# Optimization experiments

Measured on AMD Instinct MI355X. Metric: run time of the kernel, lower is better.

## Reference

```python
import jax, jax.numpy as jnp
import numpy as np

B, L, HP, H, W = 4, 32, 32, 64, 64
D, DFFN, MAXL = 32, 64, 128

def setup_inputs() -> dict:
    key = jax.random.key(0)
    ks = jax.random.split(key, 20)
    rn = lambda k, s, sc=0.1: jax.random.normal(k, s, jnp.float32) * sc
    return {
        'x': jax.random.normal(ks[0], (B, 2 * L * HP, H, W), jnp.float32),
        'in_proj_w': rn(ks[1], (D, 12)), 'in_proj_b': rn(ks[2], (D,)),
        'layer_emb': rn(ks[3], (MAXL, D)),
        'time_decay': rn(ks[4], (D,)), 'time_first': rn(ks[5], (D,)),
        'ln_tm_g': jnp.ones((D,)), 'ln_tm_b': jnp.zeros((D,)),
        'tm_r': rn(ks[6], (D, D)), 'tm_k': rn(ks[7], (D, D)),
        'tm_v': rn(ks[8], (D, D)), 'tm_out': rn(ks[9], (D, D)),
        'ln_cm_g': jnp.ones((D,)), 'ln_cm_b': jnp.zeros((D,)),
        'cm_k': rn(ks[10], (DFFN, D)), 'cm_v': rn(ks[11], (D, DFFN)), 'cm_r': rn(ks[12], (D, D)),
        'gate_w': rn(ks[13], (1, D)), 'gate_b': rn(ks[14], (1,)),
        'row_w': rn(ks[15], (H, D)), 'row_b': rn(ks[16], (H,)),
        'col_w': rn(ks[17], (W, D)), 'col_b': rn(ks[18], (W,)),
    }

def _ln(x, g, b, eps=1e-5):
    mu = x.mean(-1, keepdims=True)
    var = ((x - mu) ** 2).mean(-1, keepdims=True)
    return (x - mu) * jax.lax.rsqrt(var + eps) * g + b

def _stats(a, b):
    # a, b: [B, L, HP, H, W] -> [B, L, HP, 12]
    af = a.reshape(*a.shape[:-2], -1)
    bf = b.reshape(*b.shape[:-2], -1)
    hs = lambda f: jnp.stack([f.mean(-1), f.std(-1, ddof=1), f.min(-1), f.max(-1)], -1)
    d = af - bf
    dm = d.mean(-1, keepdims=True)
    ds = d.std(-1, ddof=1, keepdims=True)
    dl2 = jnp.linalg.norm(d, axis=-1, keepdims=True)
    na = jnp.maximum(jnp.linalg.norm(af, axis=-1), 1e-8)
    nb = jnp.maximum(jnp.linalg.norm(bf, axis=-1), 1e-8)
    cos = ((af * bf).sum(-1) / (na * nb))[..., None]
    return jnp.concatenate([hs(af), hs(bf), dm, ds, dl2, cos], -1)

def reference(x, in_proj_w, in_proj_b, layer_emb, time_decay, time_first,
              ln_tm_g, ln_tm_b, tm_r, tm_k, tm_v, tm_out,
              ln_cm_g, ln_cm_b, cm_k, cm_v, cm_r,
              gate_w, gate_b, row_w, row_b, col_w, col_b):
    n = L * HP
    a = x[:, :n].reshape(B, L, HP, H, W)
    b = x[:, n:].reshape(B, L, HP, H, W)
    stats = _stats(a, b)                                   # [B,L,HP,12]
    feat_in = jnp.einsum('blhs,ds->blhd', stats, in_proj_w) + in_proj_b \
        + layer_emb[:L][None, :, None, :]
    feat_in = jnp.transpose(feat_in, (1, 0, 2, 3))         # [L,B,HP,D]
    wdec = jnp.exp(time_decay)

    def step(state, f):
        aa, bb, pp = state
        xn = _ln(f, ln_tm_g, ln_tm_b)
        r = jax.nn.sigmoid(xn @ tm_r.T)
        k = xn @ tm_k.T
        v = xn @ tm_v.T
        ww = time_first + k
        p = jnp.maximum(pp, ww)
        e1 = jnp.exp(pp - p)
        e2 = jnp.exp(ww - p)
        wkv = (e1 * aa + e2 * v) / jnp.maximum(e1 * bb + e2, 1e-8)
        ww2 = pp - wdec
        p2 = jnp.maximum(ww2, k)
        e1b = jnp.exp(ww2 - p2)
        e2b = jnp.exp(k - p2)
        y = f + r * (wkv @ tm_out.T)
        xn2 = _ln(y, ln_cm_g, ln_cm_b)
        kk = jnp.square(jax.nn.relu(xn2 @ cm_k.T))
        y = y + jax.nn.sigmoid(xn2 @ cm_r.T) * (kk @ cm_v.T)
        return (e1b * aa + e2b * v, e1b * bb + e2b, p2), y

    z = jnp.zeros((B, HP, D), x.dtype)
    init = (z, z, jnp.full((B, HP, D), -1e30, x.dtype))
    _, feats = jax.lax.scan(step, init, feat_in)           # [L,B,HP,D]

    gate = feats @ gate_w.T + gate_b                       # [L,B,HP,1]
    row = feats @ row_w.T + row_b                          # [L,B,HP,H]
    col = feats @ col_w.T + col_b                          # [L,B,HP,W]
    mask = jax.nn.sigmoid(gate[..., None] + row[..., None] + col[..., None, :])
    aT = jnp.transpose(a, (1, 0, 2, 3, 4))
    bT = jnp.transpose(b, (1, 0, 2, 3, 4))
    merged = mask * aT + (1.0 - mask) * bT                 # [L,B,HP,H,W]
    mixed = jnp.transpose(merged, (1, 0, 2, 3, 4)).reshape(B, n, H, W)
    return mixed, jax.nn.sigmoid(gate).mean(), mask.mean()
```

## Files before the change

### kernel.cpp

```cpp
#include <hip/hip_runtime.h>
#include <math.h>


__device__ __forceinline__ float sigf(float v) { return 1.0f / (1.0f + __expf(-v)); }

__device__ __forceinline__ float bl(float v, int l) {
    return __int_as_float(__builtin_amdgcn_readlane(__float_as_int(v), l));
}

__global__ __launch_bounds__(256) void k_stats(
    const float* __restrict__ x, const float* __restrict__ in_proj_w,
    const float* __restrict__ in_proj_b, const float* __restrict__ layer_emb,
    float* __restrict__ feat)
{
    __shared__ float red[4][9];
    __shared__ float tot[9];
    const int bid = blockIdx.x;
    const int hp = bid & 31, l = (bid >> 5) & 31, bb = bid >> 10;
    const float4* pa = (const float4*)(x + (size_t)(bb * 2048 + l * 32 + hp) * 4096);
    const float4* pb = (const float4*)(x + (size_t)(bb * 2048 + 1024 + l * 32 + hp) * 4096);
    const int t = threadIdx.x;

    float sa = 0.f, saa = 0.f, sb = 0.f, sbb = 0.f, sab = 0.f;
    float mna = 3.4e38f, mxa = -3.4e38f, mnb = 3.4e38f, mxb = -3.4e38f;
#pragma unroll
    for (int it = 0; it < 4; ++it) {
        float4 a4 = pa[t + it * 256];
        float4 b4 = pb[t + it * 256];
        sa  += a4.x + a4.y + a4.z + a4.w;
        sb  += b4.x + b4.y + b4.z + b4.w;
        saa += a4.x * a4.x + a4.y * a4.y + a4.z * a4.z + a4.w * a4.w;
        sbb += b4.x * b4.x + b4.y * b4.y + b4.z * b4.z + b4.w * b4.w;
        sab += a4.x * b4.x + a4.y * b4.y + a4.z * b4.z + a4.w * b4.w;
        mna = fminf(mna, fminf(fminf(a4.x, a4.y), fminf(a4.z, a4.w)));
        mxa = fmaxf(mxa, fmaxf(fmaxf(a4.x, a4.y), fmaxf(a4.z, a4.w)));
        mnb = fminf(mnb, fminf(fminf(b4.x, b4.y), fminf(b4.z, b4.w)));
        mxb = fmaxf(mxb, fmaxf(fmaxf(b4.x, b4.y), fmaxf(b4.z, b4.w)));
    }
#pragma unroll
    for (int m = 1; m < 64; m <<= 1) {
        sa  += __shfl_xor(sa, m);
        saa += __shfl_xor(saa, m);
        sb  += __shfl_xor(sb, m);
        sbb += __shfl_xor(sbb, m);
        sab += __shfl_xor(sab, m);
        mna = fminf(mna, __shfl_xor(mna, m));
        mxa = fmaxf(mxa, __shfl_xor(mxa, m));
        mnb = fminf(mnb, __shfl_xor(mnb, m));
        mxb = fmaxf(mxb, __shfl_xor(mxb, m));
    }
    const int lane = t & 63, wv = t >> 6;
    if (lane == 0) {
        red[wv][0] = sa;  red[wv][1] = saa; red[wv][2] = sb;  red[wv][3] = sbb;
        red[wv][4] = sab; red[wv][5] = mna; red[wv][6] = mxa; red[wv][7] = mnb;
        red[wv][8] = mxb;
    }
    __syncthreads();
    if (t == 0) {
#pragma unroll
        for (int q = 0; q < 5; ++q) tot[q] = red[0][q] + red[1][q] + red[2][q] + red[3][q];
        tot[5] = fminf(fminf(red[0][5], red[1][5]), fminf(red[2][5], red[3][5]));
        tot[6] = fmaxf(fmaxf(red[0][6], red[1][6]), fmaxf(red[2][6], red[3][6]));
        tot[7] = fminf(fminf(red[0][7], red[1][7]), fminf(red[2][7], red[3][7]));
        tot[8] = fmaxf(fmaxf(red[0][8], red[1][8]), fmaxf(red[2][8], red[3][8]));
    }
    __syncthreads();
    if (t < 32) {
        const float SA = tot[0], SAA = tot[1], SB = tot[2], SBB = tot[3], SAB = tot[4];
        const float inv_n = 1.f / 4096.f, inv_nm1 = 1.f / 4095.f;
        float st[12];
        st[0] = SA * inv_n;
        st[1] = sqrtf(fmaxf(SAA - SA * SA * inv_n, 0.f) * inv_nm1);
        st[2] = tot[5]; st[3] = tot[6];
        st[4] = SB * inv_n;
        st[5] = sqrtf(fmaxf(SBB - SB * SB * inv_n, 0.f) * inv_nm1);
        st[6] = tot[7]; st[7] = tot[8];
        const float SD = SA - SB, SDD = SAA - 2.f * SAB + SBB;
        st[8]  = SD * inv_n;
        st[9]  = sqrtf(fmaxf(SDD - SD * SD * inv_n, 0.f) * inv_nm1);
        st[10] = sqrtf(fmaxf(SDD, 0.f));
        const float na = fmaxf(sqrtf(SAA), 1e-8f), nb2 = fmaxf(sqrtf(SBB), 1e-8f);
        st[11] = SAB / (na * nb2);
        float acc = in_proj_b[t] + layer_emb[l * 32 + t];
#pragma unroll
        for (int s2 = 0; s2 < 12; ++s2) acc += st[s2] * in_proj_w[t * 12 + s2];
        feat[((l * 4 + bb) * 32 + hp) * 32 + t] = acc;
    }
}

__global__ __launch_bounds__(64, 1) void k_scan(
    const float* __restrict__ feat,
    const float* __restrict__ time_decay, const float* __restrict__ time_first,
    const float* __restrict__ ln_tm_g, const float* __restrict__ ln_tm_b,
    const float* __restrict__ tm_r, const float* __restrict__ tm_k,
    const float* __restrict__ tm_v, const float* __restrict__ tm_out,
    const float* __restrict__ ln_cm_g, const float* __restrict__ ln_cm_b,
    const float* __restrict__ cm_k, const float* __restrict__ cm_v,
    const float* __restrict__ cm_r, float* __restrict__ feats_out)
{
    const int t = threadIdx.x;
    const int d = t & 31;

    float w_r[32], w_k[32], w_v[32], w_o[32], w_cr[32], w_ck[32], w_cv[64];
    {
        const float4* pr = (const float4*)(tm_r  + d * 32);
        const float4* pk = (const float4*)(tm_k  + d * 32);
        const float4* pv = (const float4*)(tm_v  + d * 32);
        const float4* po = (const float4*)(tm_out + d * 32);
        const float4* pc = (const float4*)(cm_r  + d * 32);
        const float4* pq = (const float4*)(cm_k  + t * 32);
        const float4* pw = (const float4*)(cm_v  + d * 64);
#pragma unroll
        for (int jq = 0; jq < 8; ++jq) {
            float4 v;
            v = pr[jq]; w_r[4*jq] = v.x; w_r[4*jq+1] = v.y; w_r[4*jq+2] = v.z; w_r[4*jq+3] = v.w;
            v = pk[jq]; w_k[4*jq] = v.x; w_k[4*jq+1] = v.y; w_k[4*jq+2] = v.z; w_k[4*jq+3] = v.w;
            v = pv[jq]; w_v[4*jq] = v.x; w_v[4*jq+1] = v.y; w_v[4*jq+2] = v.z; w_v[4*jq+3] = v.w;
            v = po[jq]; w_o[4*jq] = v.x; w_o[4*jq+1] = v.y; w_o[4*jq+2] = v.z; w_o[4*jq+3] = v.w;
            v = pc[jq]; w_cr[4*jq] = v.x; w_cr[4*jq+1] = v.y; w_cr[4*jq+2] = v.z; w_cr[4*jq+3] = v.w;
            v = pq[jq]; w_ck[4*jq] = v.x; w_ck[4*jq+1] = v.y; w_ck[4*jq+2] = v.z; w_ck[4*jq+3] = v.w;
        }
#pragma unroll
        for (int jq = 0; jq < 16; ++jq) {
            float4 v = pw[jq];
            w_cv[4*jq] = v.x; w_cv[4*jq+1] = v.y; w_cv[4*jq+2] = v.z; w_cv[4*jq+3] = v.w;
        }
    }
    const float gt = ln_tm_g[d], bt = ln_tm_b[d];
    const float gc = ln_cm_g[d], bc = ln_cm_b[d];
    const float tf = time_first[d];
    const float wd = __expf(time_decay[d]);
    const int seq = blockIdx.x;
    const int bb = seq >> 5, hp = seq & 31;
    const int base = (bb * 32 + hp) * 32 + d;

    float aa = 0.f, bbs = 0.f, pp = -1e30f;
    float f = feat[base];

    for (int l = 0; l < 32; ++l) {
        float fnext = 0.f;
        if (l < 31) fnext = feat[base + (l + 1) * 4096];
        float s = f, q = f * f;
#pragma unroll
        for (int m = 1; m < 32; m <<= 1) { s += __shfl_xor(s, m, 32); q += __shfl_xor(q, m, 32); }
        const float mu = s * (1.f / 32.f);
        const float var = fmaxf(q * (1.f / 32.f) - mu * mu, 0.f);
        const float xn = (f - mu) * rsqrtf(var + 1e-5f) * gt + bt;
        float racc = 0.f, kacc = 0.f, vacc = 0.f;
#pragma unroll
        for (int j = 0; j < 32; ++j) {
            const float xj = bl(xn, j);
            racc += xj * w_r[j];
            kacc += xj * w_k[j];
            vacc += xj * w_v[j];
        }
        const float r = sigf(racc);
        const float k = kacc, v = vacc;
        const float ww = tf + k;
        const float p = fmaxf(pp, ww);
        const float e1 = __expf(pp - p), e2 = __expf(ww - p);
        const float wkv = (e1 * aa + e2 * v) / fmaxf(e1 * bbs + e2, 1e-8f);
        const float ww2 = pp - wd;
        const float p2 = fmaxf(ww2, k);
        const float e1b = __expf(ww2 - p2), e2b = __expf(k - p2);
        aa = e1b * aa + e2b * v;
        bbs = e1b * bbs + e2b;
        pp = p2;
        float oacc = 0.f;
#pragma unroll
        for (int j = 0; j < 32; ++j) oacc += bl(wkv, j) * w_o[j];
        const float y = f + r * oacc;
        float s2 = y, q2 = y * y;
#pragma unroll
        for (int m = 1; m < 32; m <<= 1) { s2 += __shfl_xor(s2, m, 32); q2 += __shfl_xor(q2, m, 32); }
        const float mu2 = s2 * (1.f / 32.f);
        const float var2 = fmaxf(q2 * (1.f / 32.f) - mu2 * mu2, 0.f);
        const float xn2 = (y - mu2) * rsqrtf(var2 + 1e-5f) * gc + bc;
        float ck = 0.f, cracc = 0.f;
#pragma unroll
        for (int j = 0; j < 32; ++j) {
            const float xj = bl(xn2, j);
            ck    += xj * w_ck[j];
            cracc += xj * w_cr[j];
        }
        float kkv = fmaxf(ck, 0.f);
        kkv *= kkv;
        float cv0 = 0.f, cv1 = 0.f;
#pragma unroll
        for (int e = 0; e < 64; e += 2) {
            cv0 += bl(kkv, e)     * w_cv[e];
            cv1 += bl(kkv, e + 1) * w_cv[e + 1];
        }
        const float y2 = y + sigf(cracc) * (cv0 + cv1);
        if (t < 32) feats_out[base + l * 4096] = y2;
        f = fnext;
    }
}

__global__ __launch_bounds__(256) void k_merge(
    const float* __restrict__ x, const float* __restrict__ feats,
    const float* __restrict__ gate_w, const float* __restrict__ gate_b,
    const float* __restrict__ row_w, const float* __restrict__ row_b,
    const float* __restrict__ col_w, const float* __restrict__ col_b,
    float* __restrict__ out, float* __restrict__ gpart, float* __restrict__ mpart)
{
    __shared__ float fs[32];
    __shared__ float row_s[64], col_s[64];
    __shared__ float gate_sh;
    __shared__ float red[4];
    const int bid = blockIdx.x;
    const int hp = bid & 31, l = (bid >> 5) & 31, bb = bid >> 10;
    const int t = threadIdx.x;

    if (t < 32) fs[t] = feats[((l * 4 + bb) * 32 + hp) * 32 + t];
    __syncthreads();
    if (t < 64) {
        float acc = row_b[t];
#pragma unroll
        for (int d2 = 0; d2 < 32; ++d2) acc += fs[d2] * row_w[t * 32 + d2];
        row_s[t] = acc;
    } else if (t < 128) {
        const int w = t - 64;
        float acc = col_b[w];
#pragma unroll
        for (int d2 = 0; d2 < 32; ++d2) acc += fs[d2] * col_w[w * 32 + d2];
        col_s[w] = acc;
    } else if (t == 128) {
        float acc = gate_b[0];
#pragma unroll
        for (int d2 = 0; d2 < 32; ++d2) acc += fs[d2] * gate_w[d2];
        gate_sh = acc;
    }
    __syncthreads();
    const float gate = gate_sh;
    const float4* pa = (const float4*)(x + (size_t)(bb * 2048 + l * 32 + hp) * 4096);
    const float4* pb = (const float4*)(x + (size_t)(bb * 2048 + 1024 + l * 32 + hp) * 4096);
    float4* po = (float4*)(out + (size_t)(bb * 1024 + l * 32 + hp) * 4096);

    float msum = 0.f;
#pragma unroll
    for (int it = 0; it < 4; ++it) {
        const int i = t + it * 256;
        const float4 a4 = pa[i];
        const float4 b4 = pb[i];
        const int h = i >> 4, w0 = (i & 15) * 4;
        const float gr = gate + row_s[h];
        const float m0 = sigf(gr + col_s[w0 + 0]);
        const float m1 = sigf(gr + col_s[w0 + 1]);
        const float m2 = sigf(gr + col_s[w0 + 2]);
        const float m3 = sigf(gr + col_s[w0 + 3]);
        float4 o;
        o.x = b4.x + m0 * (a4.x - b4.x);
        o.y = b4.y + m1 * (a4.y - b4.y);
        o.z = b4.z + m2 * (a4.z - b4.z);
        o.w = b4.w + m3 * (a4.w - b4.w);
        po[i] = o;
        msum += m0 + m1 + m2 + m3;
    }
#pragma unroll
    for (int m = 1; m < 64; m <<= 1) msum += __shfl_xor(msum, m);
    if ((t & 63) == 0) red[t >> 6] = msum;
    __syncthreads();
    if (t == 0) {
        mpart[bid] = red[0] + red[1] + red[2] + red[3];
        gpart[bid] = sigf(gate);
    }
}

__global__ __launch_bounds__(256) void k_final(
    const float* __restrict__ gpart, const float* __restrict__ mpart,
    float* __restrict__ out)
{
    __shared__ float rg[4], rm[4];
    const int t = threadIdx.x;
    float gs = 0.f, ms = 0.f;
    for (int i = t; i < 4096; i += 256) { gs += gpart[i]; ms += mpart[i]; }
#pragma unroll
    for (int m = 1; m < 64; m <<= 1) { gs += __shfl_xor(gs, m); ms += __shfl_xor(ms, m); }
    if ((t & 63) == 0) { rg[t >> 6] = gs; rm[t >> 6] = ms; }
    __syncthreads();
    if (t == 0) {
        out[16777216] = (rg[0] + rg[1] + rg[2] + rg[3]) * (1.f / 4096.f);
        out[16777217] = (rm[0] + rm[1] + rm[2] + rm[3]) * (1.f / 16777216.f);
    }
}

extern "C" void kernel_launch(void* const* d_in, const int* in_sizes, int n_in,
                              void* d_out, int out_size, void* d_ws, size_t ws_size,
                              hipStream_t stream) {
    const float* x          = (const float*)d_in[0];
    const float* in_proj_w  = (const float*)d_in[1];
    const float* in_proj_b  = (const float*)d_in[2];
    const float* layer_emb  = (const float*)d_in[3];
    const float* time_decay = (const float*)d_in[4];
    const float* time_first = (const float*)d_in[5];
    const float* ln_tm_g    = (const float*)d_in[6];
    const float* ln_tm_b    = (const float*)d_in[7];
    const float* tm_r       = (const float*)d_in[8];
    const float* tm_k       = (const float*)d_in[9];
    const float* tm_v       = (const float*)d_in[10];
    const float* tm_out     = (const float*)d_in[11];
    const float* ln_cm_g    = (const float*)d_in[12];
    const float* ln_cm_b    = (const float*)d_in[13];
    const float* cm_k       = (const float*)d_in[14];
    const float* cm_v       = (const float*)d_in[15];
    const float* cm_r       = (const float*)d_in[16];
    const float* gate_w     = (const float*)d_in[17];
    const float* gate_b     = (const float*)d_in[18];
    const float* row_w      = (const float*)d_in[19];
    const float* row_b      = (const float*)d_in[20];
    const float* col_w      = (const float*)d_in[21];
    const float* col_b      = (const float*)d_in[22];
    float* out = (float*)d_out;

    float* wsf   = (float*)d_ws;
    float* feat  = wsf;
    float* fy    = wsf + 131072;
    float* gpart = wsf + 262144;
    float* mpart = wsf + 266240;

    k_stats<<<dim3(4096), dim3(256), 0, stream>>>(x, in_proj_w, in_proj_b, layer_emb, feat);
    k_scan<<<dim3(128), dim3(64), 0, stream>>>(feat, time_decay, time_first,
                                               ln_tm_g, ln_tm_b, tm_r, tm_k, tm_v, tm_out,
                                               ln_cm_g, ln_cm_b, cm_k, cm_v, cm_r, fy);
    k_merge<<<dim3(4096), dim3(256), 0, stream>>>(x, fy, gate_w, gate_b,
                                                  row_w, row_b, col_w, col_b,
                                                  out, gpart, mpart);
    k_final<<<dim3(1), dim3(256), 0, stream>>>(gpart, mpart, out);
}
```

Measured before the change: 336.5 us.

## Fuse all stages into one persistent kernel with grid-wide atomic barriers

Replaces the four launches (stats, scan, merge, final) with one persistent kernel of 256 blocks. Blocks loop over work items and synchronise through atomic-counter grid barriers, so launch gaps disappear. The scan stage now packs four sequences per block, one per wave, and splits its dot products into four independent accumulators for more ILP. The costs are fewer resident blocks for the memory-bound stats and merge phases, spin-wait barrier overhead, and an extra memset to reset the counters.

```diff
diff --git a/kernel.cpp b/kernel.cpp
--- a/kernel.cpp
+++ b/kernel.cpp
@@ -2,286 +2,334 @@
 #include <math.h>
 
 
+#define NBLK 256
+
 __device__ __forceinline__ float sigf(float v) { return 1.0f / (1.0f + __expf(-v)); }
-
 __device__ __forceinline__ float bl(float v, int l) {
     return __int_as_float(__builtin_amdgcn_readlane(__float_as_int(v), l));
 }
 
-__global__ __launch_bounds__(256) void k_stats(
+__device__ __forceinline__ void gbar(unsigned* c) {
+    __threadfence();
+    __syncthreads();
+    if (threadIdx.x == 0) {
+        __hip_atomic_fetch_add(c, 1u, __ATOMIC_ACQ_REL, __HIP_MEMORY_SCOPE_AGENT);
+        while (__hip_atomic_load(c, __ATOMIC_ACQUIRE, __HIP_MEMORY_SCOPE_AGENT) < NBLK)
+            __builtin_amdgcn_s_sleep(1);
+    }
+    __syncthreads();
+    __threadfence();
+}
+
+__global__ __launch_bounds__(256, 1) void k_fused(
     const float* __restrict__ x, const float* __restrict__ in_proj_w,
     const float* __restrict__ in_proj_b, const float* __restrict__ layer_emb,
-    float* __restrict__ feat)
-{
-    __shared__ float red[4][9];
-    __shared__ float tot[9];
-    const int bid = blockIdx.x;
-    const int hp = bid & 31, l = (bid >> 5) & 31, bb = bid >> 10;
-    const float4* pa = (const float4*)(x + (size_t)(bb * 2048 + l * 32 + hp) * 4096);
-    const float4* pb = (const float4*)(x + (size_t)(bb * 2048 + 1024 + l * 32 + hp) * 4096);
-    const int t = threadIdx.x;
-
-    float sa = 0.f, saa = 0.f, sb = 0.f, sbb = 0.f, sab = 0.f;
-    float mna = 3.4e38f, mxa = -3.4e38f, mnb = 3.4e38f, mxb = -3.4e38f;
-#pragma unroll
-    for (int it = 0; it < 4; ++it) {
-        float4 a4 = pa[t + it * 256];
-        float4 b4 = pb[t + it * 256];
-        sa  += a4.x + a4.y + a4.z + a4.w;
-        sb  += b4.x + b4.y + b4.z + b4.w;
-        saa += a4.x * a4.x + a4.y * a4.y + a4.z * a4.z + a4.w * a4.w;
-        sbb += b4.x * b4.x + b4.y * b4.y + b4.z * b4.z + b4.w * b4.w;
-        sab += a4.x * b4.x + a4.y * b4.y + a4.z * b4.z + a4.w * b4.w;
-        mna = fminf(mna, fminf(fminf(a4.x, a4.y), fminf(a4.z, a4.w)));
-        mxa = fmaxf(mxa, fmaxf(fmaxf(a4.x, a4.y), fmaxf(a4.z, a4.w)));
-        mnb = fminf(mnb, fminf(fminf(b4.x, b4.y), fminf(b4.z, b4.w)));
-        mxb = fmaxf(mxb, fmaxf(fmaxf(b4.x, b4.y), fmaxf(b4.z, b4.w)));
-    }
-#pragma unroll
-    for (int m = 1; m < 64; m <<= 1) {
-        sa  += __shfl_xor(sa, m);
-        saa += __shfl_xor(saa, m);
-        sb  += __shfl_xor(sb, m);
-        sbb += __shfl_xor(sbb, m);
-        sab += __shfl_xor(sab, m);
-        mna = fminf(mna, __shfl_xor(mna, m));
-        mxa = fmaxf(mxa, __shfl_xor(mxa, m));
-        mnb = fminf(mnb, __shfl_xor(mnb, m));
-        mxb = fmaxf(mxb, __shfl_xor(mxb, m));
-    }
-    const int lane = t & 63, wv = t >> 6;
-    if (lane == 0) {
-        red[wv][0] = sa;  red[wv][1] = saa; red[wv][2] = sb;  red[wv][3] = sbb;
-        red[wv][4] = sab; red[wv][5] = mna; red[wv][6] = mxa; red[wv][7] = mnb;
-        red[wv][8] = mxb;
-    }
-    __syncthreads();
-    if (t == 0) {
-#pragma unroll
-        for (int q = 0; q < 5; ++q) tot[q] = red[0][q] + red[1][q] + red[2][q] + red[3][q];
-        tot[5] = fminf(fminf(red[0][5], red[1][5]), fminf(red[2][5], red[3][5]));
-        tot[6] = fmaxf(fmaxf(red[0][6], red[1][6]), fmaxf(red[2][6], red[3][6]));
-        tot[7] = fminf(fminf(red[0][7], red[1][7]), fminf(red[2][7], red[3][7]));
-        tot[8] = fmaxf(fmaxf(red[0][8], red[1][8]), fmaxf(red[2][8], red[3][8]));
-    }
-    __syncthreads();
-    if (t < 32) {
-        const float SA = tot[0], SAA = tot[1], SB = tot[2], SBB = tot[3], SAB = tot[4];
-        const float inv_n = 1.f / 4096.f, inv_nm1 = 1.f / 4095.f;
-        float st[12];
-        st[0] = SA * inv_n;
-        st[1] = sqrtf(fmaxf(SAA - SA * SA * inv_n, 0.f) * inv_nm1);
-        st[2] = tot[5]; st[3] = tot[6];
-        st[4] = SB * inv_n;
-        st[5] = sqrtf(fmaxf(SBB - SB * SB * inv_n, 0.f) * inv_nm1);
-        st[6] = tot[7]; st[7] = tot[8];
-        const float SD = SA - SB, SDD = SAA - 2.f * SAB + SBB;
-        st[8]  = SD * inv_n;
-        st[9]  = sqrtf(fmaxf(SDD - SD * SD * inv_n, 0.f) * inv_nm1);
-        st[10] = sqrtf(fmaxf(SDD, 0.f));
-        const float na = fmaxf(sqrtf(SAA), 1e-8f), nb2 = fmaxf(sqrtf(SBB), 1e-8f);
-        st[11] = SAB / (na * nb2);
-        float acc = in_proj_b[t] + layer_emb[l * 32 + t];
-#pragma unroll
-        for (int s2 = 0; s2 < 12; ++s2) acc += st[s2] * in_proj_w[t * 12 + s2];
-        feat[((l * 4 + bb) * 32 + hp) * 32 + t] = acc;
-    }
-}
-
-__global__ __launch_bounds__(64, 1) void k_scan(
-    const float* __restrict__ feat,
     const float* __restrict__ time_decay, const float* __restrict__ time_first,
     const float* __restrict__ ln_tm_g, const float* __restrict__ ln_tm_b,
     const float* __restrict__ tm_r, const float* __restrict__ tm_k,
     const float* __restrict__ tm_v, const float* __restrict__ tm_out,
     const float* __restrict__ ln_cm_g, const float* __restrict__ ln_cm_b,
     const float* __restrict__ cm_k, const float* __restrict__ cm_v,
-    const float* __restrict__ cm_r, float* __restrict__ feats_out)
-{
-    const int t = threadIdx.x;
-    const int d = t & 31;
-
-    float w_r[32], w_k[32], w_v[32], w_o[32], w_cr[32], w_ck[32], w_cv[64];
-    {
-        const float4* pr = (const float4*)(tm_r  + d * 32);
-        const float4* pk = (const float4*)(tm_k  + d * 32);
-        const float4* pv = (const float4*)(tm_v  + d * 32);
-        const float4* po = (const float4*)(tm_out + d * 32);
-        const float4* pc = (const float4*)(cm_r  + d * 32);
-        const float4* pq = (const float4*)(cm_k  + t * 32);
-        const float4* pw = (const float4*)(cm_v  + d * 64);
-#pragma unroll
-        for (int jq = 0; jq < 8; ++jq) {
-            float4 v;
-            v = pr[jq]; w_r[4*jq] = v.x; w_r[4*jq+1] = v.y; w_r[4*jq+2] = v.z; w_r[4*jq+3] = v.w;
-            v = pk[jq]; w_k[4*jq] = v.x; w_k[4*jq+1] = v.y; w_k[4*jq+2] = v.z; w_k[4*jq+3] = v.w;
-            v = pv[jq]; w_v[4*jq] = v.x; w_v[4*jq+1] = v.y; w_v[4*jq+2] = v.z; w_v[4*jq+3] = v.w;
-            v = po[jq]; w_o[4*jq] = v.x; w_o[4*jq+1] = v.y; w_o[4*jq+2] = v.z; w_o[4*jq+3] = v.w;
-            v = pc[jq]; w_cr[4*jq] = v.x; w_cr[4*jq+1] = v.y; w_cr[4*jq+2] = v.z; w_cr[4*jq+3] = v.w;
-            v = pq[jq]; w_ck[4*jq] = v.x; w_ck[4*jq+1] = v.y; w_ck[4*jq+2] = v.z; w_ck[4*jq+3] = v.w;
-        }
-#pragma unroll
-        for (int jq = 0; jq < 16; ++jq) {
-            float4 v = pw[jq];
-            w_cv[4*jq] = v.x; w_cv[4*jq+1] = v.y; w_cv[4*jq+2] = v.z; w_cv[4*jq+3] = v.w;
-        }
-    }
-    const float gt = ln_tm_g[d], bt = ln_tm_b[d];
-    const float gc = ln_cm_g[d], bc = ln_cm_b[d];
-    const float tf = time_first[d];
-    const float wd = __expf(time_decay[d]);
-    const int seq = blockIdx.x;
-    const int bb = seq >> 5, hp = seq & 31;
-    const int base = (bb * 32 + hp) * 32 + d;
-
-    float aa = 0.f, bbs = 0.f, pp = -1e30f;
-    float f = feat[base];
-
-    for (int l = 0; l < 32; ++l) {
-        float fnext = 0.f;
-        if (l < 31) fnext = feat[base + (l + 1) * 4096];
-        float s = f, q = f * f;
-#pragma unroll
-        for (int m = 1; m < 32; m <<= 1) { s += __shfl_xor(s, m, 32); q += __shfl_xor(q, m, 32); }
-        const float mu = s * (1.f / 32.f);
-        const float var = fmaxf(q * (1.f / 32.f) - mu * mu, 0.f);
-        const float xn = (f - mu) * rsqrtf(var + 1e-5f) * gt + bt;
-        float racc = 0.f, kacc = 0.f, vacc = 0.f;
-#pragma unroll
-        for (int j = 0; j < 32; ++j) {
-            const float xj = bl(xn, j);
-            racc += xj * w_r[j];
-            kacc += xj * w_k[j];
-            vacc += xj * w_v[j];
-        }
-        const float r = sigf(racc);
-        const float k = kacc, v = vacc;
-        const float ww = tf + k;
-        const float p = fmaxf(pp, ww);
-        const float e1 = __expf(pp - p), e2 = __expf(ww - p);
-        const float wkv = (e1 * aa + e2 * v) / fmaxf(e1 * bbs + e2, 1e-8f);
-        const float ww2 = pp - wd;
-        const float p2 = fmaxf(ww2, k);
-        const float e1b = __expf(ww2 - p2), e2b = __expf(k - p2);
-        aa = e1b * aa + e2b * v;
-        bbs = e1b * bbs + e2b;
-        pp = p2;
-        float oacc = 0.f;
-#pragma unroll
-        for (int j = 0; j < 32; ++j) oacc += bl(wkv, j) * w_o[j];
-        const float y = f + r * oacc;
-        float s2 = y, q2 = y * y;
-#pragma unroll
-        for (int m = 1; m < 32; m <<= 1) { s2 += __shfl_xor(s2, m, 32); q2 += __shfl_xor(q2, m, 32); }
-        const float mu2 = s2 * (1.f / 32.f);
-        const float var2 = fmaxf(q2 * (1.f / 32.f) - mu2 * mu2, 0.f);
-        const float xn2 = (y - mu2) * rsqrtf(var2 + 1e-5f) * gc + bc;
-        float ck = 0.f, cracc = 0.f;
-#pragma unroll
-        for (int j = 0; j < 32; ++j) {
-            const float xj = bl(xn2, j);
-            ck    += xj * w_ck[j];
-            cracc += xj * w_cr[j];
-        }
-        float kkv = fmaxf(ck, 0.f);
-        kkv *= kkv;
-        float cv0 = 0.f, cv1 = 0.f;
-#pragma unroll
-        for (int e = 0; e < 64; e += 2) {
-            cv0 += bl(kkv, e)     * w_cv[e];
-            cv1 += bl(kkv, e + 1) * w_cv[e + 1];
-        }
-        const float y2 = y + sigf(cracc) * (cv0 + cv1);
-        if (t < 32) feats_out[base + l * 4096] = y2;
-        f = fnext;
-    }
-}
-
-__global__ __launch_bounds__(256) void k_merge(
-    const float* __restrict__ x, const float* __restrict__ feats,
+    const float* __restrict__ cm_r,
     const float* __restrict__ gate_w, const float* __restrict__ gate_b,
     const float* __restrict__ row_w, const float* __restrict__ row_b,
     const float* __restrict__ col_w, const float* __restrict__ col_b,
-    float* __restrict__ out, float* __restrict__ gpart, float* __restrict__ mpart)
+    float* __restrict__ out, float* __restrict__ wsf)
 {
-    __shared__ float fs[32];
-    __shared__ float row_s[64], col_s[64];
-    __shared__ float gate_sh;
-    __shared__ float red[4];
+    float* feat  = wsf;
+    float* fy    = wsf + 131072;
+    float* gpart = wsf + 262144;
+    float* mpart = wsf + 262400;
+    unsigned* cnt = (unsigned*)(wsf + 262656);
+
     const int bid = blockIdx.x;
-    const int hp = bid & 31, l = (bid >> 5) & 31, bb = bid >> 10;
-    const int t = threadIdx.x;
-
-    if (t < 32) fs[t] = feats[((l * 4 + bb) * 32 + hp) * 32 + t];
-    __syncthreads();
-    if (t < 64) {
-        float acc = row_b[t];
-#pragma unroll
-        for (int d2 = 0; d2 < 32; ++d2) acc += fs[d2] * row_w[t * 32 + d2];
-        row_s[t] = acc;
-    } else if (t < 128) {
-        const int w = t - 64;
-        float acc = col_b[w];
-#pragma unroll
-        for (int d2 = 0; d2 < 32; ++d2) acc += fs[d2] * col_w[w * 32 + d2];
-        col_s[w] = acc;
-    } else if (t == 128) {
-        float acc = gate_b[0];
-#pragma unroll
-        for (int d2 = 0; d2 < 32; ++d2) acc += fs[d2] * gate_w[d2];
-        gate_sh = acc;
-    }
-    __syncthreads();
-    const float gate = gate_sh;
-    const float4* pa = (const float4*)(x + (size_t)(bb * 2048 + l * 32 + hp) * 4096);
-    const float4* pb = (const float4*)(x + (size_t)(bb * 2048 + 1024 + l * 32 + hp) * 4096);
-    float4* po = (float4*)(out + (size_t)(bb * 1024 + l * 32 + hp) * 4096);
-
-    float msum = 0.f;
-#pragma unroll
-    for (int it = 0; it < 4; ++it) {
-        const int i = t + it * 256;
-        const float4 a4 = pa[i];
-        const float4 b4 = pb[i];
-        const int h = i >> 4, w0 = (i & 15) * 4;
-        const float gr = gate + row_s[h];
-        const float m0 = sigf(gr + col_s[w0 + 0]);
-        const float m1 = sigf(gr + col_s[w0 + 1]);
-        const float m2 = sigf(gr + col_s[w0 + 2]);
-        const float m3 = sigf(gr + col_s[w0 + 3]);
-        float4 o;
-        o.x = b4.x + m0 * (a4.x - b4.x);
-        o.y = b4.y + m1 * (a4.y - b4.y);
-        o.z = b4.z + m2 * (a4.z - b4.z);
-        o.w = b4.w + m3 * (a4.w - b4.w);
-        po[i] = o;
-        msum += m0 + m1 + m2 + m3;
-    }
-#pragma unroll
-    for (int m = 1; m < 64; m <<= 1) msum += __shfl_xor(msum, m);
-    if ((t & 63) == 0) red[t >> 6] = msum;
-    __syncthreads();
-    if (t == 0) {
-        mpart[bid] = red[0] + red[1] + red[2] + red[3];
-        gpart[bid] = sigf(gate);
-    }
-}
-
-__global__ __launch_bounds__(256) void k_final(
-    const float* __restrict__ gpart, const float* __restrict__ mpart,
-    float* __restrict__ out)
-{
-    __shared__ float rg[4], rm[4];
-    const int t = threadIdx.x;
-    float gs = 0.f, ms = 0.f;
-    for (int i = t; i < 4096; i += 256) { gs += gpart[i]; ms += mpart[i]; }
-#pragma unroll
-    for (int m = 1; m < 64; m <<= 1) { gs += __shfl_xor(gs, m); ms += __shfl_xor(ms, m); }
-    if ((t & 63) == 0) { rg[t >> 6] = gs; rm[t >> 6] = ms; }
-    __syncthreads();
-    if (t == 0) {
-        out[16777216] = (rg[0] + rg[1] + rg[2] + rg[3]) * (1.f / 4096.f);
-        out[16777217] = (rm[0] + rm[1] + rm[2] + rm[3]) * (1.f / 16777216.f);
+    const int t   = threadIdx.x;
+
+    {
+        __shared__ float red[4][9];
+        __shared__ float tot[9];
+        for (int it16 = 0; it16 < 16; ++it16) {
+            const int g = bid + (it16 << 8);
+            const int hp = g & 31, l = (g >> 5) & 31, bb = g >> 10;
+            const float4* pa = (const float4*)(x + (size_t)(bb * 2048 + l * 32 + hp) * 4096);
+            const float4* pb = (const float4*)(x + (size_t)(bb * 2048 + 1024 + l * 32 + hp) * 4096);
+
+            float sa = 0.f, saa = 0.f, sb = 0.f, sbb = 0.f, sab = 0.f;
+            float mna = 3.4e38f, mxa = -3.4e38f, mnb = 3.4e38f, mxb = -3.4e38f;
+#pragma unroll
+            for (int it = 0; it < 4; ++it) {
+                float4 a4 = pa[t + it * 256];
+                float4 b4 = pb[t + it * 256];
+                sa  += a4.x + a4.y + a4.z + a4.w;
+                sb  += b4.x + b4.y + b4.z + b4.w;
+                saa += a4.x * a4.x + a4.y * a4.y + a4.z * a4.z + a4.w * a4.w;
+                sbb += b4.x * b4.x + b4.y * b4.y + b4.z * b4.z + b4.w * b4.w;
+                sab += a4.x * b4.x + a4.y * b4.y + a4.z * b4.z + a4.w * b4.w;
+                mna = fminf(mna, fminf(fminf(a4.x, a4.y), fminf(a4.z, a4.w)));
+                mxa = fmaxf(mxa, fmaxf(fmaxf(a4.x, a4.y), fmaxf(a4.z, a4.w)));
+                mnb = fminf(mnb, fminf(fminf(b4.x, b4.y), fminf(b4.z, b4.w)));
+                mxb = fmaxf(mxb, fmaxf(fmaxf(b4.x, b4.y), fmaxf(b4.z, b4.w)));
+            }
+#pragma unroll
+            for (int m = 1; m < 64; m <<= 1) {
+                sa  += __shfl_xor(sa, m);
+                saa += __shfl_xor(saa, m);
+                sb  += __shfl_xor(sb, m);
+                sbb += __shfl_xor(sbb, m);
+                sab += __shfl_xor(sab, m);
+                mna = fminf(mna, __shfl_xor(mna, m));
+                mxa = fmaxf(mxa, __shfl_xor(mxa, m));
+                mnb = fminf(mnb, __shfl_xor(mnb, m));
+                mxb = fmaxf(mxb, __shfl_xor(mxb, m));
+            }
+            const int lane = t & 63, wv = t >> 6;
+            if (lane == 0) {
+                red[wv][0] = sa;  red[wv][1] = saa; red[wv][2] = sb;  red[wv][3] = sbb;
+                red[wv][4] = sab; red[wv][5] = mna; red[wv][6] = mxa; red[wv][7] = mnb;
+                red[wv][8] = mxb;
+            }
+            __syncthreads();
+            if (t == 0) {
+#pragma unroll
+                for (int q = 0; q < 5; ++q) tot[q] = red[0][q] + red[1][q] + red[2][q] + red[3][q];
+                tot[5] = fminf(fminf(red[0][5], red[1][5]), fminf(red[2][5], red[3][5]));
+                tot[6] = fmaxf(fmaxf(red[0][6], red[1][6]), fmaxf(red[2][6], red[3][6]));
+                tot[7] = fminf(fminf(red[0][7], red[1][7]), fminf(red[2][7], red[3][7]));
+                tot[8] = fmaxf(fmaxf(red[0][8], red[1][8]), fmaxf(red[2][8], red[3][8]));
+            }
+            __syncthreads();
+            if (t < 32) {
+                const float SA = tot[0], SAA = tot[1], SB = tot[2], SBB = tot[3], SAB = tot[4];
+                const float inv_n = 1.f / 4096.f, inv_nm1 = 1.f / 4095.f;
+                float st[12];
+                st[0] = SA * inv_n;
+                st[1] = sqrtf(fmaxf(SAA - SA * SA * inv_n, 0.f) * inv_nm1);
+                st[2] = tot[5]; st[3] = tot[6];
+                st[4] = SB * inv_n;
+                st[5] = sqrtf(fmaxf(SBB - SB * SB * inv_n, 0.f) * inv_nm1);
+                st[6] = tot[7]; st[7] = tot[8];
+                const float SD = SA - SB, SDD = SAA - 2.f * SAB + SBB;
+                st[8]  = SD * inv_n;
+                st[9]  = sqrtf(fmaxf(SDD - SD * SD * inv_n, 0.f) * inv_nm1);
+                st[10] = sqrtf(fmaxf(SDD, 0.f));
+                const float na = fmaxf(sqrtf(SAA), 1e-8f), nb2 = fmaxf(sqrtf(SBB), 1e-8f);
+                st[11] = SAB / (na * nb2);
+                float acc = in_proj_b[t] + layer_emb[l * 32 + t];
+#pragma unroll
+                for (int s2 = 0; s2 < 12; ++s2) acc += st[s2] * in_proj_w[t * 12 + s2];
+                feat[((l * 4 + bb) * 32 + hp) * 32 + t] = acc;
+            }
+            __syncthreads();
+        }
+    }
+    gbar(&cnt[0]);
+
+    if (bid < 32) {
+        const int lane = t & 63;
+        const int d = lane & 31;
+        const int wv = t >> 6;
+        const int seq = bid * 4 + wv;
+        const int bb = seq >> 5, hp = seq & 31;
+
+        float w_r[32], w_k[32], w_v[32], w_o[32], w_cr[32], w_ck[32], w_cv[64];
+        {
+            const float4* pr = (const float4*)(tm_r  + d * 32);
+            const float4* pk = (const float4*)(tm_k  + d * 32);
+            const float4* pv = (const float4*)(tm_v  + d * 32);
+            const float4* po = (const float4*)(tm_out + d * 32);
+            const float4* pc = (const float4*)(cm_r  + d * 32);
+            const float4* pq = (const float4*)(cm_k  + lane * 32);
+            const float4* pw = (const float4*)(cm_v  + d * 64);
+#pragma unroll
+            for (int jq = 0; jq < 8; ++jq) {
+                float4 v;
+                v = pr[jq]; w_r[4*jq] = v.x; w_r[4*jq+1] = v.y; w_r[4*jq+2] = v.z; w_r[4*jq+3] = v.w;
+                v = pk[jq]; w_k[4*jq] = v.x; w_k[4*jq+1] = v.y; w_k[4*jq+2] = v.z; w_k[4*jq+3] = v.w;
+                v = pv[jq]; w_v[4*jq] = v.x; w_v[4*jq+1] = v.y; w_v[4*jq+2] = v.z; w_v[4*jq+3] = v.w;
+                v = po[jq]; w_o[4*jq] = v.x; w_o[4*jq+1] = v.y; w_o[4*jq+2] = v.z; w_o[4*jq+3] = v.w;
+                v = pc[jq]; w_cr[4*jq] = v.x; w_cr[4*jq+1] = v.y; w_cr[4*jq+2] = v.z; w_cr[4*jq+3] = v.w;
+                v = pq[jq]; w_ck[4*jq] = v.x; w_ck[4*jq+1] = v.y; w_ck[4*jq+2] = v.z; w_ck[4*jq+3] = v.w;
+            }
+#pragma unroll
+            for (int jq = 0; jq < 16; ++jq) {
+                float4 v = pw[jq];
+                w_cv[4*jq] = v.x; w_cv[4*jq+1] = v.y; w_cv[4*jq+2] = v.z; w_cv[4*jq+3] = v.w;
+            }
+        }
+        const float gt = ln_tm_g[d], bt = ln_tm_b[d];
+        const float gc = ln_cm_g[d], bc = ln_cm_b[d];
+        const float tf = time_first[d];
+        const float wd = __expf(time_decay[d]);
+        const int base = (bb * 32 + hp) * 32 + d;
+
+        float aa = 0.f, bbs = 0.f, pp = -1e30f;
+        float f = feat[base];
+
+        for (int l = 0; l < 32; ++l) {
+            float fnext = 0.f;
+            if (l < 31) fnext = feat[base + (l + 1) * 4096];
+            float s = f, q = f * f;
+#pragma unroll
+            for (int m = 1; m < 32; m <<= 1) { s += __shfl_xor(s, m, 32); q += __shfl_xor(q, m, 32); }
+            const float mu = s * (1.f / 32.f);
+            const float var = fmaxf(q * (1.f / 32.f) - mu * mu, 0.f);
+            const float xn = (f - mu) * rsqrtf(var + 1e-5f) * gt + bt;
+            float r0 = 0.f, r1 = 0.f, r2 = 0.f, r3 = 0.f;
+            float k0 = 0.f, k1 = 0.f, k2 = 0.f, k3 = 0.f;
+            float v0 = 0.f, v1 = 0.f, v2 = 0.f, v3 = 0.f;
+#pragma unroll
+            for (int j = 0; j < 8; ++j) {
+                const float x0 = bl(xn, j), x1 = bl(xn, j + 8), x2 = bl(xn, j + 16), x3 = bl(xn, j + 24);
+                r0 += x0 * w_r[j];      r1 += x1 * w_r[j + 8];
+                r2 += x2 * w_r[j + 16]; r3 += x3 * w_r[j + 24];
+                k0 += x0 * w_k[j];      k1 += x1 * w_k[j + 8];
+                k2 += x2 * w_k[j + 16]; k3 += x3 * w_k[j + 24];
+                v0 += x0 * w_v[j];      v1 += x1 * w_v[j + 8];
+                v2 += x2 * w_v[j + 16]; v3 += x3 * w_v[j + 24];
+            }
+            const float r = sigf((r0 + r1) + (r2 + r3));
+            const float k = (k0 + k1) + (k2 + k3);
+            const float v = (v0 + v1) + (v2 + v3);
+            const float ww = tf + k;
+            const float p = fmaxf(pp, ww);
+            const float e1 = __expf(pp - p), e2 = __expf(ww - p);
+            const float wkv = (e1 * aa + e2 * v) / fmaxf(e1 * bbs + e2, 1e-8f);
+            const float ww2 = pp - wd;
+            const float p2 = fmaxf(ww2, k);
+            const float e1b = __expf(ww2 - p2), e2b = __expf(k - p2);
+            aa = e1b * aa + e2b * v;
+            bbs = e1b * bbs + e2b;
+            pp = p2;
+            float o0 = 0.f, o1 = 0.f, o2 = 0.f, o3 = 0.f;
+#pragma unroll
+            for (int j = 0; j < 8; ++j) {
+                o0 += bl(wkv, j)      * w_o[j];
+                o1 += bl(wkv, j + 8)  * w_o[j + 8];
+                o2 += bl(wkv, j + 16) * w_o[j + 16];
+                o3 += bl(wkv, j + 24) * w_o[j + 24];
+            }
+            const float y = f + r * ((o0 + o1) + (o2 + o3));
+            float s2 = y, q2 = y * y;
+#pragma unroll
+            for (int m = 1; m < 32; m <<= 1) { s2 += __shfl_xor(s2, m, 32); q2 += __shfl_xor(q2, m, 32); }
+            const float mu2 = s2 * (1.f / 32.f);
+            const float var2 = fmaxf(q2 * (1.f / 32.f) - mu2 * mu2, 0.f);
+            const float xn2 = (y - mu2) * rsqrtf(var2 + 1e-5f) * gc + bc;
+            float c0 = 0.f, c1 = 0.f, c2 = 0.f, c3 = 0.f;
+            float g0 = 0.f, g1 = 0.f, g2 = 0.f, g3 = 0.f;
+#pragma unroll
+            for (int j = 0; j < 8; ++j) {
+                const float x0 = bl(xn2, j), x1 = bl(xn2, j + 8), x2 = bl(xn2, j + 16), x3 = bl(xn2, j + 24);
+                c0 += x0 * w_ck[j];      c1 += x1 * w_ck[j + 8];
+                c2 += x2 * w_ck[j + 16]; c3 += x3 * w_ck[j + 24];
+                g0 += x0 * w_cr[j];      g1 += x1 * w_cr[j + 8];
+                g2 += x2 * w_cr[j + 16]; g3 += x3 * w_cr[j + 24];
+            }
+            float kkv = fmaxf((c0 + c1) + (c2 + c3), 0.f);
+            kkv *= kkv;
+            const float cr = sigf((g0 + g1) + (g2 + g3));
+            float u0 = 0.f, u1 = 0.f, u2 = 0.f, u3 = 0.f;
+#pragma unroll
+            for (int e = 0; e < 16; ++e) {
+                u0 += bl(kkv, e)      * w_cv[e];
+                u1 += bl(kkv, e + 16) * w_cv[e + 16];
+                u2 += bl(kkv, e + 32) * w_cv[e + 32];
+                u3 += bl(kkv, e + 48) * w_cv[e + 48];
+            }
+            const float y2 = y + cr * ((u0 + u1) + (u2 + u3));
+            if (lane < 32) fy[base + l * 4096] = y2;
+            f = fnext;
+        }
+    }
+    gbar(&cnt[1]);
+
+    {
+        __shared__ float fs[32];
+        __shared__ float row_s[64], col_s[64];
+        __shared__ float gate_sh;
+        float msum = 0.f, gsum = 0.f;
+        for (int it16 = 0; it16 < 16; ++it16) {
+            const int g = bid + (it16 << 8);
+            const int hp = g & 31, l = (g >> 5) & 31, bb = g >> 10;
+            if (t < 32) fs[t] = fy[((l * 4 + bb) * 32 + hp) * 32 + t];
+            __syncthreads();
+            if (t < 64) {
+                float a0 = row_b[t], a1 = 0.f, a2 = 0.f, a3 = 0.f;
+#pragma unroll
+                for (int d2 = 0; d2 < 8; ++d2) {
+                    a0 += fs[d2]      * row_w[t * 32 + d2];
+                    a1 += fs[d2 + 8]  * row_w[t * 32 + d2 + 8];
+                    a2 += fs[d2 + 16] * row_w[t * 32 + d2 + 16];
+                    a3 += fs[d2 + 24] * row_w[t * 32 + d2 + 24];
+                }
+                row_s[t] = (a0 + a1) + (a2 + a3);
+            } else if (t < 128) {
+                const int w = t - 64;
+                float a0 = col_b[w], a1 = 0.f, a2 = 0.f, a3 = 0.f;
+#pragma unroll
+                for (int d2 = 0; d2 < 8; ++d2) {
+                    a0 += fs[d2]      * col_w[w * 32 + d2];
+                    a1 += fs[d2 + 8]  * col_w[w * 32 + d2 + 8];
+                    a2 += fs[d2 + 16] * col_w[w * 32 + d2 + 16];
+                    a3 += fs[d2 + 24] * col_w[w * 32 + d2 + 24];
+                }
+                col_s[w] = (a0 + a1) + (a2 + a3);
+            } else if (t == 128) {
+                float acc = gate_b[0];
+#pragma unroll
+                for (int d2 = 0; d2 < 32; ++d2) acc += fs[d2] * gate_w[d2];
+                gate_sh = acc;
+            }
+            __syncthreads();
+            const float gate = gate_sh;
+            if (t == 0) gsum += sigf(gate);
+            const float4* pa = (const float4*)(x + (size_t)(bb * 2048 + l * 32 + hp) * 4096);
+            const float4* pb = (const float4*)(x + (size_t)(bb * 2048 + 1024 + l * 32 + hp) * 4096);
+            float4* po = (float4*)(out + (size_t)(bb * 1024 + l * 32 + hp) * 4096);
+#pragma unroll
+            for (int it = 0; it < 4; ++it) {
+                const int i = t + it * 256;
+                const float4 a4 = pa[i];
+                const float4 b4 = pb[i];
+                const int h = i >> 4, w0 = (i & 15) * 4;
+                const float gr = gate + row_s[h];
+                const float m0 = sigf(gr + col_s[w0 + 0]);
+                const float m1 = sigf(gr + col_s[w0 + 1]);
+                const float m2 = sigf(gr + col_s[w0 + 2]);
+                const float m3 = sigf(gr + col_s[w0 + 3]);
+                float4 o;
+                o.x = b4.x + m0 * (a4.x - b4.x);
+                o.y = b4.y + m1 * (a4.y - b4.y);
+                o.z = b4.z + m2 * (a4.z - b4.z);
+                o.w = b4.w + m3 * (a4.w - b4.w);
+                po[i] = o;
+                msum += m0 + m1 + m2 + m3;
+            }
+            __syncthreads();
+        }
+        __shared__ float red2[4];
+#pragma unroll
+        for (int m = 1; m < 64; m <<= 1) msum += __shfl_xor(msum, m);
+        if ((t & 63) == 0) red2[t >> 6] = msum;
+        __syncthreads();
+        if (t == 0) {
+            mpart[bid] = red2[0] + red2[1] + red2[2] + red2[3];
+            gpart[bid] = gsum;
+        }
+    }
+    gbar(&cnt[2]);
+
+    if (bid == 0) {
+        __shared__ float rg[4], rm[4];
+        float gs = gpart[t], ms = mpart[t];
+#pragma unroll
+        for (int m = 1; m < 64; m <<= 1) { gs += __shfl_xor(gs, m); ms += __shfl_xor(ms, m); }
+        if ((t & 63) == 0) { rg[t >> 6] = gs; rm[t >> 6] = ms; }
+        __syncthreads();
+        if (t == 0) {
+            out[16777216] = (rg[0] + rg[1] + rg[2] + rg[3]) * (1.f / 4096.f);
+            out[16777217] = (rm[0] + rm[1] + rm[2] + rm[3]) * (1.f / 16777216.f);
+        }
     }
 }
 
@@ -312,19 +360,12 @@
     const float* col_w      = (const float*)d_in[21];
     const float* col_b      = (const float*)d_in[22];
     float* out = (float*)d_out;
-
-    float* wsf   = (float*)d_ws;
-    float* feat  = wsf;
-    float* fy    = wsf + 131072;
-    float* gpart = wsf + 262144;
-    float* mpart = wsf + 266240;
-
-    k_stats<<<dim3(4096), dim3(256), 0, stream>>>(x, in_proj_w, in_proj_b, layer_emb, feat);
-    k_scan<<<dim3(128), dim3(64), 0, stream>>>(feat, time_decay, time_first,
-                                               ln_tm_g, ln_tm_b, tm_r, tm_k, tm_v, tm_out,
-                                               ln_cm_g, ln_cm_b, cm_k, cm_v, cm_r, fy);
-    k_merge<<<dim3(4096), dim3(256), 0, stream>>>(x, fy, gate_w, gate_b,
-                                                  row_w, row_b, col_w, col_b,
-                                                  out, gpart, mpart);
-    k_final<<<dim3(1), dim3(256), 0, stream>>>(gpart, mpart, out);
+    float* wsf = (float*)d_ws;
+
+    hipMemsetAsync(wsf + 262656, 0, 256, stream);
+    k_fused<<<dim3(NBLK), dim3(256), 0, stream>>>(
+        x, in_proj_w, in_proj_b, layer_emb, time_decay, time_first,
+        ln_tm_g, ln_tm_b, tm_r, tm_k, tm_v, tm_out,
+        ln_cm_g, ln_cm_b, cm_k, cm_v, cm_r,
+        gate_w, gate_b, row_w, row_b, col_w, col_b, out, wsf);
 }
```

New measurement: 531.5 us. +58.0%, slower.
